# Kernel tuning notes

Measured on AMD Instinct MI355X. Metric: run time of the kernel, lower is better.

## Reference

```python
import jax, jax.numpy as jnp
import numpy as np

B, N, IN_DIM, D, H, L = 8, 256, 2, 128, 512, 2
EPS = 1e-5


def layer_norm(x, g, b):
    m = jnp.mean(x, axis=-1, keepdims=True)
    v = jnp.var(x, axis=-1, keepdims=True)
    return (x - m) * jax.lax.rsqrt(v + EPS) * g + b


def loo_max_pool(nodes):
    # nodes: (B, N, D) -> leave-one-out max over the set axis -> (B, N, D)
    n = nodes.shape[1]
    neg = jnp.finfo(nodes.dtype).min
    mask = jnp.eye(n, dtype=bool)[None, :, :, None]          # (1, N, N, 1)
    expanded = jnp.broadcast_to(nodes[:, None, :, :],
                                (nodes.shape[0], n, n, nodes.shape[2]))
    return jnp.where(mask, neg, expanded).max(axis=2)        # (B, N, D)


def setup_inputs() -> dict:
    key = jax.random.key(0)
    ks = jax.random.split(key, 16)
    s = 0.02
    inp = {
        "x":   jax.random.normal(ks[0], (B, N, IN_DIM), dtype=jnp.float32),
        # embedding linear + its LayerNorm
        "We":  jax.random.normal(ks[1], (IN_DIM, D)) * s,
        "be":  jnp.zeros((D,), jnp.float32),
        "ge":  jnp.ones((D,), jnp.float32),
        "bge": jnp.zeros((D,), jnp.float32),
        # per-layer pool linear (concat of x and LOO-pooled context: 2D -> D)
        "Wp":  jax.random.normal(ks[2], (L, 2 * D, D)) * s,
        "bp":  jnp.zeros((L, D), jnp.float32),
        "gp":  jnp.ones((L, D), jnp.float32),
        "bgp": jnp.zeros((L, D), jnp.float32),
        # per-layer feed-forward D -> H -> D
        "W1":  jax.random.normal(ks[3], (L, D, H)) * s,
        "b1":  jnp.zeros((L, H), jnp.float32),
        "W2":  jax.random.normal(ks[4], (L, H, D)) * s,
        "b2":  jnp.zeros((L, D), jnp.float32),
        "gf":  jnp.ones((L, D), jnp.float32),
        "bgf": jnp.zeros((L, D), jnp.float32),
    }
    return inp


def reference(x, We, be, ge, bge, Wp, bp, gp, bgp, W1, b1, W2, b2, gf, bgf):
    # embeddings + embedding norm
    h = layer_norm(x @ We + be, ge, bge)                      # (B, N, D)
    for i in range(L):
        # pool layer: LOO max pooling, concat, linear, residual, norm
        pooled = loo_max_pool(h)                              # (B, N, D)
        cat = jnp.concatenate([h, pooled], axis=-1)           # (B, N, 2D)
        h = layer_norm(h + cat @ Wp[i] + bp[i], gp[i], bgp[i])
        # feed-forward, residual, norm
        ff = jax.nn.relu(h @ W1[i] + b1[i]) @ W2[i] + b2[i]
        h = layer_norm(h + ff, gf[i], bgf[i])
    return h
```

## Files before the change

kernel.cpp:

```cpp
#include <hip/hip_runtime.h>

#define BB 8
#define NN 256
#define DD 128
#define HH 512
#define LL 2
#define EPSV 1e-5f
#define TPB 4
#define BPB (NN/TPB)

__device__ __forceinline__ void waveRed2(float &a, float &b){
  #pragma unroll
  for (int off=32; off>=1; off>>=1){
    a += __shfl_xor(a, off, 64);
    b += __shfl_xor(b, off, 64);
  }
}

__device__ __forceinline__ void poolMerge(float &m1, float &m2, int &am,
                                          float o1, float o2, int oa){
  if (o1 > m1){ m2 = fmaxf(m1, o2); m1 = o1; am = oa; }
  else        { m2 = fmaxf(m2, o1); }
}

__global__ __launch_bounds__(512) void k_embed(
    const float* __restrict__ x, const float* __restrict__ We,
    const float* __restrict__ be, const float* __restrict__ ge,
    const float* __restrict__ bge, float* __restrict__ h,
    float* __restrict__ pm1p, float* __restrict__ pm2p, int* __restrict__ pargp)
{
  int tid = threadIdx.x;
  int t = tid >> 7, d = tid & 127;
  int lane = tid & 63, wid = (tid >> 6) & 1;
  int t0 = blockIdx.x * TPB;
  int tok = t0 + t;
  __shared__ float red[TPB][2][2];
  __shared__ float hf[TPB][DD];
  float x0 = x[tok*2], x1 = x[tok*2+1];
  float v = fmaf(x0, We[d], fmaf(x1, We[DD+d], be[d]));
  float s=v, q=v*v; waveRed2(s,q);
  if (lane==0){ red[t][wid][0]=s; red[t][wid][1]=q; }
  __syncthreads();
  float S=red[t][0][0]+red[t][1][0], Q=red[t][0][1]+red[t][1][1];
  float m=S*(1.f/DD), var=Q*(1.f/DD)-m*m, rs=rsqrtf(var+EPSV);
  float hv = (v-m)*rs*ge[d] + bge[d];
  h[(size_t)tok*DD + d] = hv;
  hf[t][d] = hv;
  __syncthreads();
  if (t==0){
    int b = t0 >> 8;
    int n0 = t0 & 255;
    float m1 = hf[0][d], m2 = -3.4e38f; int am = n0;
    #pragma unroll
    for (int p=1;p<TPB;++p) poolMerge(m1,m2,am, hf[p][d], -3.4e38f, n0+p);
    int blk = (t0 >> 2) & (BPB-1);
    size_t idx = ((size_t)b*BPB + blk)*DD + d;
    pm1p[idx]=m1; pm2p[idx]=m2; pargp[idx]=am;
  }
}

__global__ __launch_bounds__(512) void k_layer(
    float* __restrict__ h,
    const float* __restrict__ pm1p, const float* __restrict__ pm2p,
    const int* __restrict__ pargp,
    float* __restrict__ qm1p, float* __restrict__ qm2p, int* __restrict__ qargp,
    int write_pool,
    const float* __restrict__ Wp, const float* __restrict__ bp,
    const float* __restrict__ gp, const float* __restrict__ bgp,
    const float* __restrict__ W1, const float* __restrict__ b1,
    const float* __restrict__ W2, const float* __restrict__ b2,
    const float* __restrict__ gf, const float* __restrict__ bgf)
{
  int tid = threadIdx.x;
  int d = tid & 127, part = tid >> 7;
  int lane = tid & 63, wid = (tid >> 6) & 1;
  int t0 = blockIdx.x * TPB;
  int b = t0 >> 8;

  __shared__ float cat[TPB][2*DD];
  __shared__ float h1s[TPB][DD];
  __shared__ float us[TPB][HH];
  __shared__ float pA[4][TPB][DD];
  __shared__ float red[TPB][2][2];
  __shared__ float fm1[DD], fm2[DD];
  __shared__ int   fam[DD];
  __shared__ float sm1[4][DD], sm2[4][DD];
  __shared__ int   sam[4][DD];

  {
    size_t base = ((size_t)b*BPB + part*16)*DD + d;
    float m1 = pm1p[base], m2 = pm2p[base]; int am = pargp[base];
    #pragma unroll
    for (int i=1;i<16;++i)
      poolMerge(m1,m2,am, pm1p[base+(size_t)i*DD], pm2p[base+(size_t)i*DD],
                pargp[base+(size_t)i*DD]);
    sm1[part][d]=m1; sm2[part][d]=m2; sam[part][d]=am;
  }
  __syncthreads();
  if (part==0){
    float m1=sm1[0][d], m2=sm2[0][d]; int am=sam[0][d];
    #pragma unroll
    for (int p=1;p<4;++p) poolMerge(m1,m2,am, sm1[p][d], sm2[p][d], sam[p][d]);
    fm1[d]=m1; fm2[d]=m2; fam[d]=am;
  }
  __syncthreads();

  #pragma unroll
  for (int rep=0; rep<2; ++rep){
    int e = rep*512 + tid;
    int t = e >> 8, c = e & 255;
    int tok = t0 + t, n = (t0 & 255) + t;
    float v;
    if (c < DD) v = h[(size_t)tok*DD + c];
    else { int cc = c - DD; v = (n==fam[cc]) ? fm2[cc] : fm1[cc]; }
    cat[t][c] = v;
  }
  __syncthreads();

  float y[TPB];
  #pragma unroll
  for (int t=0;t<TPB;++t) y[t]=0.f;
  {
    const float* wp = Wp + d;
    int k0 = part*64;
    for (int k=k0; k<k0+64; k+=4){
      float w0=wp[(k+0)*DD], w1=wp[(k+1)*DD], w2=wp[(k+2)*DD], w3=wp[(k+3)*DD];
      #pragma unroll
      for (int t=0;t<TPB;++t){
        float4 c4 = *(const float4*)&cat[t][k];
        y[t]=fmaf(c4.x,w0,y[t]); y[t]=fmaf(c4.y,w1,y[t]);
        y[t]=fmaf(c4.z,w2,y[t]); y[t]=fmaf(c4.w,w3,y[t]);
      }
    }
  }
  #pragma unroll
  for (int t=0;t<TPB;++t) pA[part][t][d] = y[t];
  __syncthreads();

  {
    int t = part;
    float v = pA[0][t][d]+pA[1][t][d]+pA[2][t][d]+pA[3][t][d] + bp[d] + cat[t][d];
    float s=v,q=v*v; waveRed2(s,q);
    if (lane==0){ red[t][wid][0]=s; red[t][wid][1]=q; }
    __syncthreads();
    float S=red[t][0][0]+red[t][1][0], Q=red[t][0][1]+red[t][1][1];
    float m=S*(1.f/DD), var=Q*(1.f/DD)-m*m, rs=rsqrtf(var+EPSV);
    h1s[t][d] = (v-m)*rs*gp[d] + bgp[d];
  }
  __syncthreads();

  {
    int j = tid;
    float acc[TPB];
    float b1v = b1[j];
    #pragma unroll
    for (int t=0;t<TPB;++t) acc[t]=b1v;
    const float* w1p = W1 + j;
    for (int k=0;k<DD;k+=4){
      float w0=w1p[(k+0)*HH], w1=w1p[(k+1)*HH], w2=w1p[(k+2)*HH], w3=w1p[(k+3)*HH];
      #pragma unroll
      for (int t=0;t<TPB;++t){
        float4 h4 = *(const float4*)&h1s[t][k];
        acc[t]=fmaf(h4.x,w0,acc[t]); acc[t]=fmaf(h4.y,w1,acc[t]);
        acc[t]=fmaf(h4.z,w2,acc[t]); acc[t]=fmaf(h4.w,w3,acc[t]);
      }
    }
    #pragma unroll
    for (int t=0;t<TPB;++t) us[t][j]=fmaxf(acc[t],0.f);
  }
  __syncthreads();

  float z[TPB];
  #pragma unroll
  for (int t=0;t<TPB;++t) z[t]=0.f;
  {
    const float* w2p = W2 + d;
    int j0 = part*128;
    for (int j=j0;j<j0+128;j+=4){
      float w0=w2p[(j+0)*DD], w1=w2p[(j+1)*DD], w2v=w2p[(j+2)*DD], w3=w2p[(j+3)*DD];
      #pragma unroll
      for (int t=0;t<TPB;++t){
        float4 u4 = *(const float4*)&us[t][j];
        z[t]=fmaf(u4.x,w0,z[t]); z[t]=fmaf(u4.y,w1,z[t]);
        z[t]=fmaf(u4.z,w2v,z[t]); z[t]=fmaf(u4.w,w3,z[t]);
      }
    }
  }
  #pragma unroll
  for (int t=0;t<TPB;++t) pA[part][t][d]=z[t];
  __syncthreads();

  {
    int t = part;
    float v = pA[0][t][d]+pA[1][t][d]+pA[2][t][d]+pA[3][t][d] + b2[d] + h1s[t][d];
    float s=v,q=v*v; waveRed2(s,q);
    if (lane==0){ red[t][wid][0]=s; red[t][wid][1]=q; }
    __syncthreads();
    float S=red[t][0][0]+red[t][1][0], Q=red[t][0][1]+red[t][1][1];
    float m=S*(1.f/DD), var=Q*(1.f/DD)-m*m, rs=rsqrtf(var+EPSV);
    float hv = (v-m)*rs*gf[d] + bgf[d];
    h[(size_t)(t0+t)*DD + d] = hv;
    cat[t][d] = hv;
  }
  if (write_pool){
    __syncthreads();
    if (part==0){
      int n0 = t0 & 255;
      float m1 = cat[0][d], m2=-3.4e38f; int am=n0;
      #pragma unroll
      for (int p=1;p<TPB;++p) poolMerge(m1,m2,am, cat[p][d], -3.4e38f, n0+p);
      int blk = (t0>>2)&(BPB-1);
      size_t idx = ((size_t)b*BPB+blk)*DD + d;
      qm1p[idx]=m1; qm2p[idx]=m2; qargp[idx]=am;
    }
  }
}

extern "C" void kernel_launch(void* const* d_in, const int* in_sizes, int n_in,
                              void* d_out, int out_size, void* d_ws, size_t ws_size,
                              hipStream_t stream)
{
  const float* x   = (const float*)d_in[0];
  const float* We  = (const float*)d_in[1];
  const float* be  = (const float*)d_in[2];
  const float* ge  = (const float*)d_in[3];
  const float* bge = (const float*)d_in[4];
  const float* Wp  = (const float*)d_in[5];
  const float* bp  = (const float*)d_in[6];
  const float* gp  = (const float*)d_in[7];
  const float* bgp = (const float*)d_in[8];
  const float* W1  = (const float*)d_in[9];
  const float* b1  = (const float*)d_in[10];
  const float* W2  = (const float*)d_in[11];
  const float* b2  = (const float*)d_in[12];
  const float* gf  = (const float*)d_in[13];
  const float* bgf = (const float*)d_in[14];

  float* h = (float*)d_out;
  const size_t NSTAT = (size_t)BB*BPB*DD;
  float* pA1 = (float*)d_ws;
  float* pA2 = pA1 + NSTAT;
  int*   pAa = (int*)(pA2 + NSTAT);
  float* pB1 = (float*)(pAa + NSTAT);
  float* pB2 = pB1 + NSTAT;
  int*   pBa = (int*)(pB2 + NSTAT);

  const int grid = (BB*NN)/TPB;

  k_embed<<<grid, 512, 0, stream>>>(x, We, be, ge, bge, h, pA1, pA2, pAa);

  k_layer<<<grid, 512, 0, stream>>>(h, pA1, pA2, pAa, pB1, pB2, pBa, 1,
      Wp,                bp,        gp,        bgp,
      W1,                b1,        W2,        b2,
      gf,                bgf);

  k_layer<<<grid, 512, 0, stream>>>(h, pB1, pB2, pBa, pB1, pB2, pBa, 0,
      Wp + (size_t)2*DD*DD, bp + DD,  gp + DD,  bgp + DD,
      W1 + (size_t)DD*HH,   b1 + HH,  W2 + (size_t)HH*DD, b2 + DD,
      gf + DD,              bgf + DD);
}
```

Baseline: 128.5 us.

## Remap the three GEMV stages to float4 weight loads with split-K partial sums

Each of the three matrix stages (pool linear, W1, W2) now has every thread load a float4 of four adjacent output columns per k and accumulate four columns per token. The K dimension is split across 16 or 4 thread groups, and partials are reduced through a larger shared buffer. The aim is wider, coalesced global weight loads and fewer scalar loads per FMA. The cost is a much larger shared partial-sum array, about 32KB, which may reduce occupancy, plus extra reduction passes and syncs.

```diff
diff --git a/kernel.cpp b/kernel.cpp
--- a/kernel.cpp
+++ b/kernel.cpp
@@ -72,7 +72,8 @@
     const float* __restrict__ gf, const float* __restrict__ bgf)
 {
   int tid = threadIdx.x;
-  int d = tid & 127, part = tid >> 7;
+  int d = tid & 127;
+  int fourth = tid >> 7;
   int lane = tid & 63, wid = (tid >> 6) & 1;
   int t0 = blockIdx.x * TPB;
   int b = t0 >> 8;
@@ -80,7 +81,7 @@
   __shared__ float cat[TPB][2*DD];
   __shared__ float h1s[TPB][DD];
   __shared__ float us[TPB][HH];
-  __shared__ float pA[4][TPB][DD];
+  __shared__ float pf[16*TPB*DD];
   __shared__ float red[TPB][2][2];
   __shared__ float fm1[DD], fm2[DD];
   __shared__ int   fam[DD];
@@ -88,16 +89,16 @@
   __shared__ int   sam[4][DD];
 
   {
-    size_t base = ((size_t)b*BPB + part*16)*DD + d;
+    size_t base = ((size_t)b*BPB + fourth*16)*DD + d;
     float m1 = pm1p[base], m2 = pm2p[base]; int am = pargp[base];
     #pragma unroll
     for (int i=1;i<16;++i)
       poolMerge(m1,m2,am, pm1p[base+(size_t)i*DD], pm2p[base+(size_t)i*DD],
                 pargp[base+(size_t)i*DD]);
-    sm1[part][d]=m1; sm2[part][d]=m2; sam[part][d]=am;
-  }
-  __syncthreads();
-  if (part==0){
+    sm1[fourth][d]=m1; sm2[fourth][d]=m2; sam[fourth][d]=am;
+  }
+  __syncthreads();
+  if (fourth==0){
     float m1=sm1[0][d], m2=sm2[0][d]; int am=sam[0][d];
     #pragma unroll
     for (int p=1;p<4;++p) poolMerge(m1,m2,am, sm1[p][d], sm2[p][d], sam[p][d]);
@@ -117,29 +118,38 @@
   }
   __syncthreads();
 
-  float y[TPB];
-  #pragma unroll
-  for (int t=0;t<TPB;++t) y[t]=0.f;
-  {
-    const float* wp = Wp + d;
-    int k0 = part*64;
-    for (int k=k0; k<k0+64; k+=4){
-      float w0=wp[(k+0)*DD], w1=wp[(k+1)*DD], w2=wp[(k+2)*DD], w3=wp[(k+3)*DD];
+  {
+    int q = tid & 31, p = tid >> 5;
+    float4 acc[TPB];
+    #pragma unroll
+    for (int t=0;t<TPB;++t) acc[t] = make_float4(0.f,0.f,0.f,0.f);
+    const float* wp = Wp + 4*q;
+    int k0 = p*16;
+    #pragma unroll
+    for (int kk=0; kk<16; ++kk){
+      int k = k0 + kk;
+      float4 w = *(const float4*)&wp[k*DD];
       #pragma unroll
       for (int t=0;t<TPB;++t){
-        float4 c4 = *(const float4*)&cat[t][k];
-        y[t]=fmaf(c4.x,w0,y[t]); y[t]=fmaf(c4.y,w1,y[t]);
-        y[t]=fmaf(c4.z,w2,y[t]); y[t]=fmaf(c4.w,w3,y[t]);
+        float c = cat[t][k];
+        acc[t].x = fmaf(c, w.x, acc[t].x);
+        acc[t].y = fmaf(c, w.y, acc[t].y);
+        acc[t].z = fmaf(c, w.z, acc[t].z);
+        acc[t].w = fmaf(c, w.w, acc[t].w);
       }
     }
-  }
-  #pragma unroll
-  for (int t=0;t<TPB;++t) pA[part][t][d] = y[t];
-  __syncthreads();
-
-  {
-    int t = part;
-    float v = pA[0][t][d]+pA[1][t][d]+pA[2][t][d]+pA[3][t][d] + bp[d] + cat[t][d];
+    #pragma unroll
+    for (int t=0;t<TPB;++t)
+      *(float4*)&pf[((p*TPB)+t)*DD + 4*q] = acc[t];
+  }
+  __syncthreads();
+
+  {
+    int t = fourth;
+    float v = 0.f;
+    #pragma unroll
+    for (int p=0;p<16;++p) v += pf[((p*TPB)+t)*DD + d];
+    v += bp[d] + cat[t][d];
     float s=v,q=v*v; waveRed2(s,q);
     if (lane==0){ red[t][wid][0]=s; red[t][wid][1]=q; }
     __syncthreads();
@@ -150,49 +160,76 @@
   __syncthreads();
 
   {
+    int J = tid & 127, p = tid >> 7;
+    float4 acc[TPB];
+    #pragma unroll
+    for (int t=0;t<TPB;++t) acc[t] = make_float4(0.f,0.f,0.f,0.f);
+    const float* w1p = W1 + 4*J;
+    int k0 = p*32;
+    #pragma unroll
+    for (int kk=0; kk<32; ++kk){
+      int k = k0 + kk;
+      float4 w = *(const float4*)&w1p[k*HH];
+      #pragma unroll
+      for (int t=0;t<TPB;++t){
+        float c = h1s[t][k];
+        acc[t].x = fmaf(c, w.x, acc[t].x);
+        acc[t].y = fmaf(c, w.y, acc[t].y);
+        acc[t].z = fmaf(c, w.z, acc[t].z);
+        acc[t].w = fmaf(c, w.w, acc[t].w);
+      }
+    }
+    #pragma unroll
+    for (int t=0;t<TPB;++t)
+      *(float4*)&pf[((p*TPB)+t)*HH + 4*J] = acc[t];
+  }
+  __syncthreads();
+
+  {
     int j = tid;
-    float acc[TPB];
     float b1v = b1[j];
     #pragma unroll
-    for (int t=0;t<TPB;++t) acc[t]=b1v;
-    const float* w1p = W1 + j;
-    for (int k=0;k<DD;k+=4){
-      float w0=w1p[(k+0)*HH], w1=w1p[(k+1)*HH], w2=w1p[(k+2)*HH], w3=w1p[(k+3)*HH];
+    for (int t=0;t<TPB;++t){
+      float v = pf[((0*TPB)+t)*HH + j] + pf[((1*TPB)+t)*HH + j]
+              + pf[((2*TPB)+t)*HH + j] + pf[((3*TPB)+t)*HH + j];
+      us[t][j] = fmaxf(v + b1v, 0.f);
+    }
+  }
+  __syncthreads();
+
+  {
+    int q = tid & 31, p = tid >> 5;
+    float4 acc[TPB];
+    #pragma unroll
+    for (int t=0;t<TPB;++t) acc[t] = make_float4(0.f,0.f,0.f,0.f);
+    const float* w2p = W2 + 4*q;
+    int j0 = p*32;
+    #pragma unroll
+    for (int jj=0; jj<32; ++jj){
+      int j = j0 + jj;
+      float4 w = *(const float4*)&w2p[j*DD];
       #pragma unroll
       for (int t=0;t<TPB;++t){
-        float4 h4 = *(const float4*)&h1s[t][k];
-        acc[t]=fmaf(h4.x,w0,acc[t]); acc[t]=fmaf(h4.y,w1,acc[t]);
-        acc[t]=fmaf(h4.z,w2,acc[t]); acc[t]=fmaf(h4.w,w3,acc[t]);
+        float c = us[t][j];
+        acc[t].x = fmaf(c, w.x, acc[t].x);
+        acc[t].y = fmaf(c, w.y, acc[t].y);
+        acc[t].z = fmaf(c, w.z, acc[t].z);
+        acc[t].w = fmaf(c, w.w, acc[t].w);
       }
     }
-    #pragma unroll
-    for (int t=0;t<TPB;++t) us[t][j]=fmaxf(acc[t],0.f);
-  }
-  __syncthreads();
-
-  float z[TPB];
-  #pragma unroll
-  for (int t=0;t<TPB;++t) z[t]=0.f;
-  {
-    const float* w2p = W2 + d;
-    int j0 = part*128;
-    for (int j=j0;j<j0+128;j+=4){
-      float w0=w2p[(j+0)*DD], w1=w2p[(j+1)*DD], w2v=w2p[(j+2)*DD], w3=w2p[(j+3)*DD];
-      #pragma unroll
-      for (int t=0;t<TPB;++t){
-        float4 u4 = *(const float4*)&us[t][j];
-        z[t]=fmaf(u4.x,w0,z[t]); z[t]=fmaf(u4.y,w1,z[t]);
-        z[t]=fmaf(u4.z,w2v,z[t]); z[t]=fmaf(u4.w,w3,z[t]);
-      }
-    }
-  }
-  #pragma unroll
-  for (int t=0;t<TPB;++t) pA[part][t][d]=z[t];
-  __syncthreads();
-
-  {
-    int t = part;
-    float v = pA[0][t][d]+pA[1][t][d]+pA[2][t][d]+pA[3][t][d] + b2[d] + h1s[t][d];
+    __syncthreads();
+    #pragma unroll
+    for (int t=0;t<TPB;++t)
+      *(float4*)&pf[((p*TPB)+t)*DD + 4*q] = acc[t];
+  }
+  __syncthreads();
+
+  {
+    int t = fourth;
+    float v = 0.f;
+    #pragma unroll
+    for (int p=0;p<16;++p) v += pf[((p*TPB)+t)*DD + d];
+    v += b2[d] + h1s[t][d];
     float s=v,q=v*v; waveRed2(s,q);
     if (lane==0){ red[t][wid][0]=s; red[t][wid][1]=q; }
     __syncthreads();
@@ -204,7 +241,7 @@
   }
   if (write_pool){
     __syncthreads();
-    if (part==0){
+    if (fourth==0){
       int n0 = t0 & 255;
       float m1 = cat[0][d], m2=-3.4e38f; int am=n0;
       #pragma unroll
```

Result: slower. 133.3 us (+3.7%).

## Use bf16 MFMA matmuls with pre-transposed weights and 8 tokens per block

Applied to the files above, without the earlier changes.

Adds a conversion kernel that transposes and casts Wp, W1 and W2 to bf16. The layer kernel then computes all three matmuls with 16x16x32 bf16 MFMA instructions instead of scalar fp32 FMAs, and tokens per block grow from 4 to 8. The MFMA M dimension of 16 is padded, so half of each tile is idle. LayerNorm is restructured so one wave handles one token. The aim is to remove the fp32 FMA compute and the repeated weight loads, at the cost of bf16 precision loss and an extra launch on every call.

```diff
diff --git a/kernel.cpp b/kernel.cpp
--- a/kernel.cpp
+++ b/kernel.cpp
@@ -1,4 +1,5 @@
 #include <hip/hip_runtime.h>
+#include <hip/hip_bf16.h>
 
 #define BB 8
 #define NN 256
@@ -6,8 +7,19 @@
 #define HH 512
 #define LL 2
 #define EPSV 1e-5f
-#define TPB 4
-#define BPB (NN/TPB)
+#define TPE 4
+#define TPB 8
+#define BPE (NN/TPE)
+#define BPL (NN/TPB)
+
+typedef unsigned short ushort_t;
+typedef __attribute__((ext_vector_type(8))) short bf16x8;
+typedef __attribute__((ext_vector_type(4))) float f32x4;
+
+__device__ __forceinline__ ushort_t f2b(float v){
+  __hip_bfloat16 h = __float2bfloat16(v);
+  return *(ushort_t*)&h;
+}
 
 __device__ __forceinline__ void waveRed2(float &a, float &b){
   #pragma unroll
@@ -21,6 +33,38 @@
                                           float o1, float o2, int oa){
   if (o1 > m1){ m2 = fmaxf(m1, o2); m1 = o1; am = oa; }
   else        { m2 = fmaxf(m2, o1); }
+}
+
+__global__ __launch_bounds__(256) void k_conv(
+    const float* __restrict__ Wp, const float* __restrict__ W1,
+    const float* __restrict__ W2, ushort_t* __restrict__ wpT,
+    ushort_t* __restrict__ w1T, ushort_t* __restrict__ w2T)
+{
+  __shared__ float tile[32][33];
+  int bid = blockIdx.x;
+  const float* src; ushort_t* dst; int K, N, kt, nt;
+  if (bid < 64){
+    int l = bid >> 5, r = bid & 31;
+    src = Wp + (size_t)l*256*128; dst = wpT + (size_t)l*128*256;
+    K=256; N=128; kt = r >> 2; nt = r & 3;
+  } else if (bid < 192){
+    int e = bid - 64; int l = e >> 6, r = e & 63;
+    src = W1 + (size_t)l*128*512; dst = w1T + (size_t)l*512*128;
+    K=128; N=512; kt = r >> 4; nt = r & 15;
+  } else {
+    int e = bid - 192; int l = e >> 6, r = e & 63;
+    src = W2 + (size_t)l*512*128; dst = w2T + (size_t)l*128*512;
+    K=512; N=128; kt = r >> 2; nt = r & 3;
+  }
+  int k0 = kt*32, n0 = nt*32;
+  int tx = threadIdx.x & 31, ty = threadIdx.x >> 5;
+  #pragma unroll
+  for (int i=0;i<4;++i)
+    tile[ty + i*8][tx] = src[(size_t)(k0+ty+i*8)*N + n0 + tx];
+  __syncthreads();
+  #pragma unroll
+  for (int i=0;i<4;++i)
+    dst[(size_t)(n0+ty+i*8)*K + k0 + tx] = f2b(tile[tx][ty + i*8]);
 }
 
 __global__ __launch_bounds__(512) void k_embed(
@@ -32,10 +76,10 @@
   int tid = threadIdx.x;
   int t = tid >> 7, d = tid & 127;
   int lane = tid & 63, wid = (tid >> 6) & 1;
-  int t0 = blockIdx.x * TPB;
+  int t0 = blockIdx.x * TPE;
   int tok = t0 + t;
-  __shared__ float red[TPB][2][2];
-  __shared__ float hf[TPB][DD];
+  __shared__ float red[TPE][2][2];
+  __shared__ float hf[TPE][DD];
   float x0 = x[tok*2], x1 = x[tok*2+1];
   float v = fmaf(x0, We[d], fmaf(x1, We[DD+d], be[d]));
   float s=v, q=v*v; waveRed2(s,q);
@@ -52,9 +96,9 @@
     int n0 = t0 & 255;
     float m1 = hf[0][d], m2 = -3.4e38f; int am = n0;
     #pragma unroll
-    for (int p=1;p<TPB;++p) poolMerge(m1,m2,am, hf[p][d], -3.4e38f, n0+p);
-    int blk = (t0 >> 2) & (BPB-1);
-    size_t idx = ((size_t)b*BPB + blk)*DD + d;
+    for (int p=1;p<TPE;++p) poolMerge(m1,m2,am, hf[p][d], -3.4e38f, n0+p);
+    int blk = (t0 >> 2) & (BPE-1);
+    size_t idx = ((size_t)b*BPE + blk)*DD + d;
     pm1p[idx]=m1; pm2p[idx]=m2; pargp[idx]=am;
   }
 }
@@ -62,42 +106,45 @@
 __global__ __launch_bounds__(512) void k_layer(
     float* __restrict__ h,
     const float* __restrict__ pm1p, const float* __restrict__ pm2p,
-    const int* __restrict__ pargp,
+    const int* __restrict__ pargp, int npart,
     float* __restrict__ qm1p, float* __restrict__ qm2p, int* __restrict__ qargp,
     int write_pool,
-    const float* __restrict__ Wp, const float* __restrict__ bp,
+    const ushort_t* __restrict__ WpT, const float* __restrict__ bp,
     const float* __restrict__ gp, const float* __restrict__ bgp,
-    const float* __restrict__ W1, const float* __restrict__ b1,
-    const float* __restrict__ W2, const float* __restrict__ b2,
+    const ushort_t* __restrict__ W1T, const float* __restrict__ b1,
+    const ushort_t* __restrict__ W2T, const float* __restrict__ b2,
     const float* __restrict__ gf, const float* __restrict__ bgf)
 {
   int tid = threadIdx.x;
-  int d = tid & 127, part = tid >> 7;
-  int lane = tid & 63, wid = (tid >> 6) & 1;
+  int d = tid & 127, fourth = tid >> 7;
+  int wv = tid >> 6;
+  int lane = tid & 63;
+  int m = lane & 15, q = lane >> 4;
   int t0 = blockIdx.x * TPB;
   int b = t0 >> 8;
 
-  __shared__ float cat[TPB][2*DD];
-  __shared__ float h1s[TPB][DD];
-  __shared__ float us[TPB][HH];
-  __shared__ float pA[4][TPB][DD];
-  __shared__ float red[TPB][2][2];
-  __shared__ float fm1[DD], fm2[DD];
-  __shared__ int   fam[DD];
-  __shared__ float sm1[4][DD], sm2[4][DD];
-  __shared__ int   sam[4][DD];
-
-  {
-    size_t base = ((size_t)b*BPB + part*16)*DD + d;
+  __shared__ ushort_t catb[16*256];
+  __shared__ float    hres[8*128];
+  __shared__ float    sA[16*128];
+  __shared__ ushort_t h1b[16*128];
+  __shared__ float    h1f[8*128];
+  __shared__ ushort_t ub[16*512];
+  __shared__ float fm1[128], fm2[128];
+  __shared__ int   fam[128];
+  __shared__ float sm1[4][128], sm2[4][128];
+  __shared__ int   sam[4][128];
+
+  {
+    int per = npart >> 2;
+    size_t base = ((size_t)b*npart + fourth*per)*DD + d;
     float m1 = pm1p[base], m2 = pm2p[base]; int am = pargp[base];
-    #pragma unroll
-    for (int i=1;i<16;++i)
+    for (int i=1;i<per;++i)
       poolMerge(m1,m2,am, pm1p[base+(size_t)i*DD], pm2p[base+(size_t)i*DD],
                 pargp[base+(size_t)i*DD]);
-    sm1[part][d]=m1; sm2[part][d]=m2; sam[part][d]=am;
-  }
-  __syncthreads();
-  if (part==0){
+    sm1[fourth][d]=m1; sm2[fourth][d]=m2; sam[fourth][d]=am;
+  }
+  __syncthreads();
+  if (fourth==0){
     float m1=sm1[0][d], m2=sm2[0][d]; int am=sam[0][d];
     #pragma unroll
     for (int p=1;p<4;++p) poolMerge(m1,m2,am, sm1[p][d], sm2[p][d], sam[p][d]);
@@ -106,111 +153,111 @@
   __syncthreads();
 
   #pragma unroll
-  for (int rep=0; rep<2; ++rep){
+  for (int rep=0; rep<4; ++rep){
     int e = rep*512 + tid;
     int t = e >> 8, c = e & 255;
     int tok = t0 + t, n = (t0 & 255) + t;
     float v;
-    if (c < DD) v = h[(size_t)tok*DD + c];
+    if (c < DD){ v = h[(size_t)tok*DD + c]; hres[t*128 + c] = v; }
     else { int cc = c - DD; v = (n==fam[cc]) ? fm2[cc] : fm1[cc]; }
-    cat[t][c] = v;
-  }
-  __syncthreads();
-
-  float y[TPB];
-  #pragma unroll
-  for (int t=0;t<TPB;++t) y[t]=0.f;
-  {
-    const float* wp = Wp + d;
-    int k0 = part*64;
-    for (int k=k0; k<k0+64; k+=4){
-      float w0=wp[(k+0)*DD], w1=wp[(k+1)*DD], w2=wp[(k+2)*DD], w3=wp[(k+3)*DD];
+    catb[t*256 + c] = f2b(v);
+  }
+  __syncthreads();
+
+  {
+    int n0 = wv*16;
+    f32x4 acc = {0.f,0.f,0.f,0.f};
+    const ushort_t* ap = catb + m*256 + q*8;
+    const ushort_t* wp = WpT + (size_t)(n0+m)*256 + q*8;
+    #pragma unroll
+    for (int ks=0; ks<8; ++ks){
+      bf16x8 af = *(const bf16x8*)(ap + ks*32);
+      bf16x8 wf = *(const bf16x8*)(wp + ks*32);
+      acc = __builtin_amdgcn_mfma_f32_16x16x32_bf16(af, wf, acc, 0,0,0);
+    }
+    #pragma unroll
+    for (int r=0;r<4;++r) sA[(q*4+r)*128 + n0 + m] = acc[r];
+  }
+  __syncthreads();
+
+  {
+    int t = wv, g = lane;
+    float2 v2 = *(const float2*)&sA[t*128 + 2*g];
+    float v0 = v2.x + bp[2*g]   + hres[t*128 + 2*g];
+    float v1 = v2.y + bp[2*g+1] + hres[t*128 + 2*g + 1];
+    float s = v0+v1, qq = v0*v0 + v1*v1;
+    waveRed2(s,qq);
+    float mean = s*(1.f/128), var = qq*(1.f/128) - mean*mean;
+    float rs = rsqrtf(var + EPSV);
+    float o0 = (v0-mean)*rs*gp[2*g]   + bgp[2*g];
+    float o1 = (v1-mean)*rs*gp[2*g+1] + bgp[2*g+1];
+    unsigned pk = (unsigned)f2b(o0) | ((unsigned)f2b(o1) << 16);
+    *(unsigned*)&h1b[t*128 + 2*g] = pk;
+    *(float2*)&h1f[t*128 + 2*g] = make_float2(o0, o1);
+  }
+  __syncthreads();
+
+  {
+    const ushort_t* ap = h1b + m*128 + q*8;
+    #pragma unroll
+    for (int i=0;i<4;++i){
+      int n0 = i*128 + wv*16;
+      f32x4 acc = {0.f,0.f,0.f,0.f};
+      const ushort_t* wp = W1T + (size_t)(n0+m)*128 + q*8;
       #pragma unroll
-      for (int t=0;t<TPB;++t){
-        float4 c4 = *(const float4*)&cat[t][k];
-        y[t]=fmaf(c4.x,w0,y[t]); y[t]=fmaf(c4.y,w1,y[t]);
-        y[t]=fmaf(c4.z,w2,y[t]); y[t]=fmaf(c4.w,w3,y[t]);
+      for (int ks=0; ks<4; ++ks){
+        bf16x8 af = *(const bf16x8*)(ap + ks*32);
+        bf16x8 wf = *(const bf16x8*)(wp + ks*32);
+        acc = __builtin_amdgcn_mfma_f32_16x16x32_bf16(af, wf, acc, 0,0,0);
       }
+      float bb = b1[n0+m];
+      #pragma unroll
+      for (int r=0;r<4;++r)
+        ub[(q*4+r)*512 + n0 + m] = f2b(fmaxf(acc[r] + bb, 0.f));
     }
   }
-  #pragma unroll
-  for (int t=0;t<TPB;++t) pA[part][t][d] = y[t];
-  __syncthreads();
-
-  {
-    int t = part;
-    float v = pA[0][t][d]+pA[1][t][d]+pA[2][t][d]+pA[3][t][d] + bp[d] + cat[t][d];
-    float s=v,q=v*v; waveRed2(s,q);
-    if (lane==0){ red[t][wid][0]=s; red[t][wid][1]=q; }
-    __syncthreads();
-    float S=red[t][0][0]+red[t][1][0], Q=red[t][0][1]+red[t][1][1];
-    float m=S*(1.f/DD), var=Q*(1.f/DD)-m*m, rs=rsqrtf(var+EPSV);
-    h1s[t][d] = (v-m)*rs*gp[d] + bgp[d];
-  }
-  __syncthreads();
-
-  {
-    int j = tid;
-    float acc[TPB];
-    float b1v = b1[j];
-    #pragma unroll
-    for (int t=0;t<TPB;++t) acc[t]=b1v;
-    const float* w1p = W1 + j;
-    for (int k=0;k<DD;k+=4){
-      float w0=w1p[(k+0)*HH], w1=w1p[(k+1)*HH], w2=w1p[(k+2)*HH], w3=w1p[(k+3)*HH];
-      #pragma unroll
-      for (int t=0;t<TPB;++t){
-        float4 h4 = *(const float4*)&h1s[t][k];
-        acc[t]=fmaf(h4.x,w0,acc[t]); acc[t]=fmaf(h4.y,w1,acc[t]);
-        acc[t]=fmaf(h4.z,w2,acc[t]); acc[t]=fmaf(h4.w,w3,acc[t]);
-      }
+  __syncthreads();
+
+  {
+    int n0 = wv*16;
+    f32x4 acc = {0.f,0.f,0.f,0.f};
+    const ushort_t* ap = ub + m*512 + q*8;
+    const ushort_t* wp = W2T + (size_t)(n0+m)*512 + q*8;
+    #pragma unroll
+    for (int ks=0; ks<16; ++ks){
+      bf16x8 af = *(const bf16x8*)(ap + ks*32);
+      bf16x8 wf = *(const bf16x8*)(wp + ks*32);
+      acc = __builtin_amdgcn_mfma_f32_16x16x32_bf16(af, wf, acc, 0,0,0);
     }
     #pragma unroll
-    for (int t=0;t<TPB;++t) us[t][j]=fmaxf(acc[t],0.f);
-  }
-  __syncthreads();
-
-  float z[TPB];
-  #pragma unroll
-  for (int t=0;t<TPB;++t) z[t]=0.f;
-  {
-    const float* w2p = W2 + d;
-    int j0 = part*128;
-    for (int j=j0;j<j0+128;j+=4){
-      float w0=w2p[(j+0)*DD], w1=w2p[(j+1)*DD], w2v=w2p[(j+2)*DD], w3=w2p[(j+3)*DD];
-      #pragma unroll
-      for (int t=0;t<TPB;++t){
-        float4 u4 = *(const float4*)&us[t][j];
-        z[t]=fmaf(u4.x,w0,z[t]); z[t]=fmaf(u4.y,w1,z[t]);
-        z[t]=fmaf(u4.z,w2v,z[t]); z[t]=fmaf(u4.w,w3,z[t]);
-      }
-    }
-  }
-  #pragma unroll
-  for (int t=0;t<TPB;++t) pA[part][t][d]=z[t];
-  __syncthreads();
-
-  {
-    int t = part;
-    float v = pA[0][t][d]+pA[1][t][d]+pA[2][t][d]+pA[3][t][d] + b2[d] + h1s[t][d];
-    float s=v,q=v*v; waveRed2(s,q);
-    if (lane==0){ red[t][wid][0]=s; red[t][wid][1]=q; }
-    __syncthreads();
-    float S=red[t][0][0]+red[t][1][0], Q=red[t][0][1]+red[t][1][1];
-    float m=S*(1.f/DD), var=Q*(1.f/DD)-m*m, rs=rsqrtf(var+EPSV);
-    float hv = (v-m)*rs*gf[d] + bgf[d];
-    h[(size_t)(t0+t)*DD + d] = hv;
-    cat[t][d] = hv;
+    for (int r=0;r<4;++r) sA[(q*4+r)*128 + n0 + m] = acc[r];
+  }
+  __syncthreads();
+
+  {
+    int t = wv, g = lane;
+    float2 v2 = *(const float2*)&sA[t*128 + 2*g];
+    float v0 = v2.x + b2[2*g]   + h1f[t*128 + 2*g];
+    float v1 = v2.y + b2[2*g+1] + h1f[t*128 + 2*g + 1];
+    float s = v0+v1, qq = v0*v0 + v1*v1;
+    waveRed2(s,qq);
+    float mean = s*(1.f/128), var = qq*(1.f/128) - mean*mean;
+    float rs = rsqrtf(var + EPSV);
+    float o0 = (v0-mean)*rs*gf[2*g]   + bgf[2*g];
+    float o1 = (v1-mean)*rs*gf[2*g+1] + bgf[2*g+1];
+    *(float2*)&h[(size_t)(t0+t)*DD + 2*g] = make_float2(o0, o1);
+    *(float2*)&hres[t*128 + 2*g] = make_float2(o0, o1);
   }
   if (write_pool){
     __syncthreads();
-    if (part==0){
+    if (tid < 128){
       int n0 = t0 & 255;
-      float m1 = cat[0][d], m2=-3.4e38f; int am=n0;
+      float m1 = hres[tid], m2 = -3.4e38f; int am = n0;
       #pragma unroll
-      for (int p=1;p<TPB;++p) poolMerge(m1,m2,am, cat[p][d], -3.4e38f, n0+p);
-      int blk = (t0>>2)&(BPB-1);
-      size_t idx = ((size_t)b*BPB+blk)*DD + d;
+      for (int p=1;p<TPB;++p)
+        poolMerge(m1,m2,am, hres[p*128 + tid], -3.4e38f, n0+p);
+      int blk = (t0 >> 3) & (BPL-1);
+      size_t idx = ((size_t)b*BPL + blk)*DD + tid;
       qm1p[idx]=m1; qm2p[idx]=m2; qargp[idx]=am;
     }
   }
@@ -237,25 +284,32 @@
   const float* bgf = (const float*)d_in[14];
 
   float* h = (float*)d_out;
-  const size_t NSTAT = (size_t)BB*BPB*DD;
-  float* pA1 = (float*)d_ws;
-  float* pA2 = pA1 + NSTAT;
-  int*   pAa = (int*)(pA2 + NSTAT);
-  float* pB1 = (float*)(pAa + NSTAT);
-  float* pB2 = pB1 + NSTAT;
-  int*   pBa = (int*)(pB2 + NSTAT);
-
-  const int grid = (BB*NN)/TPB;
-
-  k_embed<<<grid, 512, 0, stream>>>(x, We, be, ge, bge, h, pA1, pA2, pAa);
-
-  k_layer<<<grid, 512, 0, stream>>>(h, pA1, pA2, pAa, pB1, pB2, pBa, 1,
-      Wp,                bp,        gp,        bgp,
-      W1,                b1,        W2,        b2,
-      gf,                bgf);
-
-  k_layer<<<grid, 512, 0, stream>>>(h, pB1, pB2, pBa, pB1, pB2, pBa, 0,
-      Wp + (size_t)2*DD*DD, bp + DD,  gp + DD,  bgp + DD,
-      W1 + (size_t)DD*HH,   b1 + HH,  W2 + (size_t)HH*DD, b2 + DD,
-      gf + DD,              bgf + DD);
-}
+  char* ws = (char*)d_ws;
+  const size_t NA = (size_t)BB*BPE*DD;
+  const size_t NB = (size_t)BB*BPL*DD;
+  float* pA1 = (float*)ws;                    ws += NA*4;
+  float* pA2 = (float*)ws;                    ws += NA*4;
+  int*   pAa = (int*)ws;                      ws += NA*4;
+  float* pB1 = (float*)ws;                    ws += NB*4;
+  float* pB2 = (float*)ws;                    ws += NB*4;
+  int*   pBa = (int*)ws;                      ws += NB*4;
+  ushort_t* wpT = (ushort_t*)ws;              ws += (size_t)LL*DD*2*DD*2;
+  ushort_t* w1T = (ushort_t*)ws;              ws += (size_t)LL*HH*DD*2;
+  ushort_t* w2T = (ushort_t*)ws;              ws += (size_t)LL*DD*HH*2;
+
+  k_conv<<<320, 256, 0, stream>>>(Wp, W1, W2, wpT, w1T, w2T);
+
+  k_embed<<<(BB*NN)/TPE, 512, 0, stream>>>(x, We, be, ge, bge, h, pA1, pA2, pAa);
+
+  k_layer<<<(BB*NN)/TPB, 512, 0, stream>>>(h, pA1, pA2, pAa, BPE,
+      pB1, pB2, pBa, 1,
+      wpT,                     bp,       gp,       bgp,
+      w1T,                     b1,       w2T,      b2,
+      gf,                      bgf);
+
+  k_layer<<<(BB*NN)/TPB, 512, 0, stream>>>(h, pB1, pB2, pBa, BPL,
+      pB1, pB2, pBa, 0,
+      wpT + (size_t)DD*2*DD,   bp + DD,  gp + DD,  bgp + DD,
+      w1T + (size_t)HH*DD,     b1 + HH,  w2T + (size_t)DD*HH, b2 + DD,
+      gf + DD,                 bgf + DD);
+}
```

Result: faster. 123.2 us (-4.1%).
